# Performance work log

Measured on AMD Instinct MI355X. Metric: run time of the kernel, lower is better.

## Reference

```python
import jax, jax.numpy as jnp
import numpy as np

NTOKEN, EMBED, HID, VDIM, MAXLEN = 15000, 1024, 1024, 2048, 20
B, NOBJ = 128, 36

def gru_cell(x, h, Wih, Whh, bih, bhh):
    gi = x @ Wih.T + bih
    gh = h @ Whh.T + bhh
    i_r, i_z, i_n = jnp.split(gi, 3, axis=-1)
    h_r, h_z, h_n = jnp.split(gh, 3, axis=-1)
    r = jax.nn.sigmoid(i_r + h_r)
    z = jax.nn.sigmoid(i_z + h_z)
    n = jnp.tanh(i_n + r * h_n)
    return (1.0 - z) * n + z * h

def setup_inputs() -> dict:
    key = jax.random.key(0)
    ks = jax.random.split(key, 20)
    s = 0.02
    inp = {
        'v': jax.random.normal(ks[0], (B, NOBJ, VDIM), jnp.float32),
        'caption': jax.random.randint(ks[1], (B, MAXLEN), 0, NTOKEN, jnp.int32),
        'cap_len': jax.random.randint(ks[2], (B,), 2, MAXLEN + 1, jnp.int32),
        'emb': jax.random.normal(ks[3], (NTOKEN, EMBED), jnp.float32) * s,
        'Wih1': jax.random.normal(ks[4], (3 * HID, HID + VDIM + EMBED), jnp.float32) * s,
        'Whh1': jax.random.normal(ks[5], (3 * HID, HID), jnp.float32) * s,
        'bih1': jnp.zeros((3 * HID,), jnp.float32),
        'bhh1': jnp.zeros((3 * HID,), jnp.float32),
        'Wih2': jax.random.normal(ks[6], (3 * HID, VDIM + HID), jnp.float32) * s,
        'Whh2': jax.random.normal(ks[7], (3 * HID, HID), jnp.float32) * s,
        'bih2': jnp.zeros((3 * HID,), jnp.float32),
        'bhh2': jnp.zeros((3 * HID,), jnp.float32),
        'Wfc1': jax.random.normal(ks[8], (HID, HID), jnp.float32) * s,
        'bfc1': jnp.zeros((HID,), jnp.float32),
        'Wfc2': jax.random.normal(ks[9], (NTOKEN, HID), jnp.float32) * s,
        'bfc2': jnp.zeros((NTOKEN,), jnp.float32),
        'Wv': jax.random.normal(ks[10], (HID, VDIM), jnp.float32) * s,
        'bv': jnp.zeros((HID,), jnp.float32),
        'Wq': jax.random.normal(ks[11], (HID, HID), jnp.float32) * s,
        'bq': jnp.zeros((HID,), jnp.float32),
        'Wa': jax.random.normal(ks[12], (1, HID), jnp.float32) * s,
        'ba': jnp.zeros((1,), jnp.float32),
    }
    return inp

def reference(v, caption, cap_len, emb, Wih1, Whh1, bih1, bhh1, Wih2, Whh2, bih2, bhh2,
              Wfc1, bfc1, Wfc2, bfc2, Wv, bv, Wq, bq, Wa, ba):
    batch, num_objs, _ = v.shape
    # sort by descending caption length (stable, matching torch sort + inverse perm)
    sort_id = jnp.argsort(-cap_len)
    restore_id = jnp.argsort(sort_id)
    cap_len_s = cap_len[sort_id]
    sort_caption = caption[sort_id]
    v_s = v[sort_id]
    v_mean = v_s.mean(axis=1)                      # [B, VDIM]
    cap_emb = emb[sort_caption]                    # [B, T, E]
    # precompute attention v-projection (relu FCNet): [B, O, HID]
    v_proj = jax.nn.relu(jnp.einsum('bod,hd->boh', v_s, Wv) + bv)
    dec_len = cap_len_s - 1
    T = cap_emb.shape[1] - 1                       # max_len - 1 decode steps
    ts = jnp.arange(T)
    mask = (ts[:, None] < dec_len[None, :])        # [T, B]
    cap_seq = jnp.swapaxes(cap_emb[:, :T, :], 0, 1)  # [T, B, E]

    def step(carry, xs):
        h1, h2 = carry
        cap_t, m_t = xs
        x1 = jnp.concatenate([h2, v_mean, cap_t], axis=1)
        h1 = gru_cell(x1, h1, Wih1, Whh1, bih1, bhh1)
        h = h1 @ Wfc1.T + bfc1
        q_proj = jax.nn.relu(h @ Wq.T + bq)        # [B, HID]
        joint = v_proj * q_proj[:, None, :]        # [B, O, HID]
        logits = jnp.einsum('boh,h->bo', joint, Wa[0]) + ba[0]
        att = jax.nn.softmax(logits, axis=1)       # [B, O]
        att_v = jnp.einsum('bo,bod->bd', att, v_s)
        h2 = gru_cell(jnp.concatenate([att_v, h], axis=1), h2, Wih2, Whh2, bih2, bhh2)
        out_t = h2 @ Wfc2.T + bfc2                 # [B, NTOKEN]
        out_t = jnp.where(m_t[:, None], out_t, 0.0)
        alpha_t = jnp.where(m_t[:, None], att, 0.0)
        return (h1, h2), (out_t, alpha_t)

    h0 = jnp.zeros((batch, HID), v.dtype)
    (_, _), (outs, alphas) = jax.lax.scan(step, (h0, h0), (cap_seq, mask))
    # pad last timestep (loop never reaches t = max_len-1) and softmax all rows
    output = jnp.concatenate([jnp.swapaxes(outs, 0, 1),
                              jnp.zeros((batch, 1, Wfc2.shape[0]), v.dtype)], axis=1)
    alpha = jnp.concatenate([jnp.swapaxes(alphas, 0, 1),
                             jnp.zeros((batch, 1, num_objs), v.dtype)], axis=1)
    predict = jax.nn.softmax(output, axis=2)[restore_id]
    return predict, sort_caption[:, 1:], alpha[restore_id]
```

## Files before the change

kernel.cpp:

```cpp
#include <hip/hip_runtime.h>
#include <math.h>

#define NTOKEN 15000
#define EMBED  1024
#define HID    1024
#define VDIM   2048
#define MAXLEN 20
#define BATCH  128
#define NOBJ   36
#define TSTEP  19

typedef unsigned short ushort_t;
typedef __attribute__((ext_vector_type(8))) short short8;
typedef __attribute__((ext_vector_type(4))) float floatx4;

__device__ __forceinline__ float b2f(ushort_t u) {
    return __uint_as_float(((unsigned)u) << 16);
}
__device__ __forceinline__ ushort_t f2b(float f) {
    unsigned x = __float_as_uint(f);
    unsigned r = (x + 0x7fffu + ((x >> 16) & 1u)) >> 16;
    return (ushort_t)r;
}

template<int NF, bool OUT_BF16>
__device__ __forceinline__ void mfma_core(
    ushort_t* As, ushort_t* Bs,
    const ushort_t* __restrict__ A, int lda, const int* __restrict__ arow,
    const ushort_t* __restrict__ B, int ldb,
    void* __restrict__ Cv, int ldc, const int* __restrict__ crow,
    const float* __restrict__ bias, const float* __restrict__ mulvec,
    const float* __restrict__ cadd, long ldadd, int cadd_div,
    int relu_n, int N, int K, int m0, int n0, int k0)
{
    constexpr int ABUF = 128 * 40;
    constexpr int BBUF = NF * 16 * 40;
    const int tid  = threadIdx.x;
    const int lane = tid & 63;
    const int w    = tid >> 6;

    floatx4 acc[2][NF];
#pragma unroll
    for (int mf = 0; mf < 2; mf++)
#pragma unroll
        for (int nf = 0; nf < NF; nf++) acc[mf][nf] = (floatx4){0.f, 0.f, 0.f, 0.f};

    const int a_r = tid >> 1;
    const int a_c = (tid & 1) * 16;
    int a_g = m0 + a_r;
    if (arow) a_g = arow[a_g];
    const ushort_t* Aptr = A + (long)a_g * lda + k0 + a_c;

    int b_r, b_c;
    if constexpr (NF == 8)      { b_r = tid >> 1; b_c = (tid & 1) * 16; }
    else if constexpr (NF == 4) { b_r = tid >> 2; b_c = (tid & 3) * 8; }
    else                        { b_r = tid >> 3; b_c = (tid & 7) * 4; }
    int b_g = n0 + b_r;
    if (b_g >= N) b_g = N - 1;
    const ushort_t* Bptr = B + (long)b_g * ldb + k0 + b_c;

    const int fr = lane & 15;
    const int q8 = (lane >> 4) * 8;

    auto LDB = [&](uint4& v0, uint4& v1, int kof) {
        if constexpr (NF == 8) {
            v0 = *(const uint4*)(Bptr + kof);
            v1 = *(const uint4*)(Bptr + kof + 8);
        } else if constexpr (NF == 4) {
            v0 = *(const uint4*)(Bptr + kof);
        } else {
            uint2 t2 = *(const uint2*)(Bptr + kof);
            v0.x = t2.x; v0.y = t2.y;
        }
    };
    auto STA = [&](ushort_t* Asb, const uint4& v0, const uint4& v1) {
        *(uint4*)(Asb + a_r * 40 + a_c)     = v0;
        *(uint4*)(Asb + a_r * 40 + a_c + 8) = v1;
    };
    auto STB = [&](ushort_t* Bsb, const uint4& v0, const uint4& v1) {
        if constexpr (NF == 8) {
            *(uint4*)(Bsb + b_r * 40 + b_c)     = v0;
            *(uint4*)(Bsb + b_r * 40 + b_c + 8) = v1;
        } else if constexpr (NF == 4) {
            *(uint4*)(Bsb + b_r * 40 + b_c) = v0;
        } else {
            *(uint2*)(Bsb + b_r * 40 + b_c) = make_uint2(v0.x, v0.y);
        }
    };
    auto CMP = [&](const ushort_t* Asb, const ushort_t* Bsb) {
        short8 bfr[NF];
#pragma unroll
        for (int nf = 0; nf < NF; nf++)
            bfr[nf] = *(const short8*)(Bsb + (nf * 16 + fr) * 40 + q8);
#pragma unroll
        for (int mf = 0; mf < 2; mf++) {
            short8 af = *(const short8*)(Asb + (w * 32 + mf * 16 + fr) * 40 + q8);
#pragma unroll
            for (int nf = 0; nf < NF; nf++)
                acc[mf][nf] = __builtin_amdgcn_mfma_f32_16x16x32_bf16(
                    af, bfr[nf], acc[mf][nf], 0, 0, 0);
        }
    };

    const int T = K >> 5;

    uint4 ae0, ae1, ao0, ao1;
    uint4 be0, be1, bo0, bo1;
    ae0 = *(const uint4*)(Aptr);       ae1 = *(const uint4*)(Aptr + 8);
    LDB(be0, be1, 0);
    ao0 = *(const uint4*)(Aptr + 32);  ao1 = *(const uint4*)(Aptr + 40);
    LDB(bo0, bo1, 32);
    STA(As, ae0, ae1); STB(Bs, be0, be1);
    if (T > 2) {
        ae0 = *(const uint4*)(Aptr + 64); ae1 = *(const uint4*)(Aptr + 72);
        LDB(be0, be1, 64);
    }
    __syncthreads();

    for (int i = 0; i < T; i += 2) {
        STA(As + ABUF, ao0, ao1); STB(Bs + BBUF, bo0, bo1);
        if (i + 3 < T) {
            int kof = (i + 3) * 32;
            ao0 = *(const uint4*)(Aptr + kof); ao1 = *(const uint4*)(Aptr + kof + 8);
            LDB(bo0, bo1, kof);
        }
        CMP(As, Bs);
        __syncthreads();
        if (i + 2 < T) {
            STA(As, ae0, ae1); STB(Bs, be0, be1);
            if (i + 4 < T) {
                int kof = (i + 4) * 32;
                ae0 = *(const uint4*)(Aptr + kof); ae1 = *(const uint4*)(Aptr + kof + 8);
                LDB(be0, be1, kof);
            }
        }
        CMP(As + ABUF, Bs + BBUF);
        __syncthreads();
    }

    const int rq = lane >> 4;
#pragma unroll
    for (int mf = 0; mf < 2; mf++) {
#pragma unroll
        for (int r = 0; r < 4; r++) {
            int m = m0 + w * 32 + mf * 16 + rq * 4 + r;
            int cm = crow ? crow[m] : m;
            const float* caddrow = cadd ? (cadd + (long)(m / cadd_div) * ldadd) : nullptr;
#pragma unroll
            for (int nf = 0; nf < NF; nf++) {
                int n = n0 + nf * 16 + fr;
                if (n < N) {
                    float val = acc[mf][nf][r];
                    if (bias)    val += bias[n];
                    if (caddrow) val += caddrow[n];
                    if (n < relu_n) val = fmaxf(val, 0.f);
                    if (mulvec)  val *= mulvec[n];
                    if (OUT_BF16) ((ushort_t*)Cv)[(long)cm * ldc + n] = f2b(val);
                    else          ((float*)Cv)[(long)cm * ldc + n]   = val;
                }
            }
        }
    }
}

template<int NF, bool OUT_BF16>
__global__ __launch_bounds__(256) void mfma_gemm(
    const ushort_t* __restrict__ A, int lda, const int* __restrict__ arow,
    const ushort_t* __restrict__ B, int ldb,
    void* __restrict__ C, int ldc, const int* __restrict__ crow,
    const float* __restrict__ bias, const float* __restrict__ mulvec,
    const float* __restrict__ cadd, long ldadd, int cadd_div,
    int relu_n, int N, int K, int swz)
{
    __shared__ ushort_t As[2 * 128 * 40];
    __shared__ ushort_t Bs[2 * NF * 16 * 40];
    int mt = blockIdx.y, nt = blockIdx.x;
    if (swz) {
        int D = gridDim.x * gridDim.y;
        int d = blockIdx.y * gridDim.x + blockIdx.x;
        int x = d & 7, j = d >> 3, q = D >> 3, r = D & 7;
        int g = x * q + (x < r ? x : r) + j;
        mt = g % gridDim.y; nt = g / gridDim.y;
    }
    mfma_core<NF, OUT_BF16>(As, Bs, A, lda, arow, B, ldb, C, ldc, crow,
                            bias, mulvec, cadd, ldadd, cadd_div, relu_n,
                            N, K, mt * 128, nt * (NF * 16), 0);
}

template<int NF, int KS>
__global__ __launch_bounds__(256) void splitk_gemm(
    const ushort_t* __restrict__ A, int lda,
    const ushort_t* __restrict__ B, int ldb,
    float* __restrict__ C0, float* __restrict__ CP, long pstride, int ldc,
    const float* __restrict__ bias,
    const float* __restrict__ cadd, long ldadd,
    int N, int K)
{
    __shared__ ushort_t As[2 * 128 * 40];
    __shared__ ushort_t Bs[2 * NF * 16 * 40];
    const int s = blockIdx.y;
    const int Kc = K / KS;
    float* C = (s == 0) ? C0 : (CP + (long)(s - 1) * pstride);
    mfma_core<NF, false>(As, Bs, A, lda, nullptr, B, ldb, C, ldc, nullptr,
                         s == 0 ? bias : nullptr, nullptr,
                         s == 0 ? cadd : nullptr, ldadd, 1,
                         0, N, Kc, 0, blockIdx.x * (NF * 16), s * Kc);
}

template<int NF, int KS>
__global__ __launch_bounds__(256) void step3_kernel(
    const ushort_t* __restrict__ h1b, const ushort_t* __restrict__ h2b,
    const ushort_t* __restrict__ Wih1h, const ushort_t* __restrict__ Whh1b,
    const ushort_t* __restrict__ Whh2b,
    float* __restrict__ gi, float* __restrict__ gh, float* __restrict__ gh2,
    float* __restrict__ P_gi, float* __restrict__ P_gh, float* __restrict__ P_gh2,
    const float* __restrict__ gi1s_t,
    const float* __restrict__ bhh1, const float* __restrict__ bhh2)
{
    __shared__ ushort_t As[2 * 128 * 40];
    __shared__ ushort_t Bs[2 * NF * 16 * 40];
    const int s = blockIdx.y;
    const int Kc = 1024 / KS;
    const ushort_t* A; const ushort_t* B; float* C0; float* CP;
    const float* bias = nullptr; const float* cadd = nullptr;
    if (blockIdx.z == 0)      { A = h2b; B = Wih1h; C0 = gi;  CP = P_gi;  cadd = gi1s_t; }
    else if (blockIdx.z == 1) { A = h1b; B = Whh1b; C0 = gh;  CP = P_gh;  bias = bhh1; }
    else                      { A = h2b; B = Whh2b; C0 = gh2; CP = P_gh2; bias = bhh2; }
    float* C = (s == 0) ? C0 : (CP + (long)(s - 1) * 393216);
    mfma_core<NF, false>(As, Bs, A, 1024, nullptr, B, 1024, C, 3072, nullptr,
                         s == 0 ? bias : nullptr, nullptr,
                         s == 0 ? cadd : nullptr, (long)TSTEP * 3072, 1, 0,
                         3072, Kc, 0, blockIdx.x * (NF * 16), s * Kc);
}

__global__ void init_kernel(const int* __restrict__ caption,
                            int* __restrict__ tok_idx, int* __restrict__ crow20,
                            float* __restrict__ h12f, ushort_t* __restrict__ h12b)
{
    int idx = blockIdx.x * 256 + threadIdx.x;
    if (idx < BATCH * TSTEP) {
        int b = idx / TSTEP, t = idx % TSTEP;
        tok_idx[idx] = caption[b * MAXLEN + t];
        crow20[idx]  = b * MAXLEN + t;
    }
    h12f[idx] = 0.f;
    h12b[idx] = 0;
}

__global__ void sort_caption_kernel(const int* __restrict__ caption,
                                    const int* __restrict__ cap_len,
                                    float* __restrict__ out1)
{
    int i = threadIdx.x;
    if (i < BATCH) {
        int li = cap_len[i];
        int rank = 0;
        for (int j = 0; j < BATCH; j++) {
            int lj = cap_len[j];
            if (lj > li || (lj == li && j < i)) rank++;
        }
        for (int k = 0; k < TSTEP; k++)
            out1[rank * TSTEP + k] = (float)caption[i * MAXLEN + 1 + k];
    }
}

__global__ void vmean_kernel(const float* __restrict__ v,
                             float* __restrict__ vmean, ushort_t* __restrict__ vmeanb)
{
    int idx = blockIdx.x * 256 + threadIdx.x;
    int b = idx >> 11, d = idx & (VDIM - 1);
    float s = 0.f;
    for (int o = 0; o < NOBJ; o++) s += v[((long)b * NOBJ + o) * VDIM + d];
    float m = s * (1.0f / 36.0f);
    vmean[idx] = m;
    vmeanb[idx] = f2b(m);
}

__global__ void conv_kernel(const float* __restrict__ src, long ld,
                            const int* __restrict__ rowidx,
                            ushort_t* __restrict__ dst, int rows, int cols)
{
    long idx4 = ((long)blockIdx.x * 256 + threadIdx.x) * 4;
    if (idx4 >= (long)rows * cols) return;
    int r = (int)(idx4 / cols);
    int c = (int)(idx4 % cols);
    long sr = rowidx ? rowidx[r] : r;
    float4 f = *(const float4*)(src + sr * ld + c);
    dst[idx4 + 0] = f2b(f.x);
    dst[idx4 + 1] = f2b(f.y);
    dst[idx4 + 2] = f2b(f.z);
    dst[idx4 + 3] = f2b(f.w);
}

__global__ void transpose_conv_kernel(const float* __restrict__ src,
                                      ushort_t* __restrict__ dst)
{
    __shared__ float tile[32][33];
    int bx = blockIdx.x, by = blockIdx.y;
    int lx = threadIdx.x & 31, ly = threadIdx.x >> 5;
    for (int i = 0; i < 32; i += 8)
        tile[ly + i][lx] = src[(long)(by * 32 + ly + i) * 1024 + bx * 32 + lx];
    __syncthreads();
    for (int i = 0; i < 32; i += 8)
        dst[(long)(bx * 32 + ly + i) * 1024 + by * 32 + lx] = f2b(tile[lx][ly + i]);
}

__global__ void bias_fold_kernel(const float* __restrict__ Wq,
                                 const float* __restrict__ Wih2,
                                 const float* __restrict__ bfc1,
                                 const float* __restrict__ bq,
                                 const float* __restrict__ bih2,
                                 float* __restrict__ bcat2)
{
    int wave = blockIdx.x * 4 + (threadIdx.x >> 6);
    int lane = threadIdx.x & 63;
    for (int n = wave; n < 4096; n += 256) {
        const float* wrow = (n < 1024) ? (Wq + (long)n * 1024)
                                       : (Wih2 + (long)(n - 1024) * 3072 + 2048);
        float s = 0.f;
        for (int j = lane; j < 1024; j += 64) s += wrow[j] * bfc1[j];
        for (int off = 32; off > 0; off >>= 1) s += __shfl_down(s, off);
        if (lane == 0) bcat2[n] = s + ((n < 1024) ? bq[n] : bih2[n - 1024]);
    }
}

__global__ void gru_kernel(const float* __restrict__ gi, const float* __restrict__ giP,
                           const float* __restrict__ gh, const float* __restrict__ ghP,
                           int nsp,
                           float* __restrict__ h, ushort_t* __restrict__ hb,
                           ushort_t* __restrict__ hstore, int t)
{
    int idx = blockIdx.x * 256 + threadIdx.x;
    int b = idx >> 10, j = idx & (HID - 1);
    long o0 = (long)b * 3 * HID + j;
    float ir = gi[o0], iz = gi[o0 + HID], in_ = gi[o0 + 2 * HID];
    float hr = gh[o0], hz = gh[o0 + HID], hn  = gh[o0 + 2 * HID];
    for (int s = 0; s < nsp; s++) {
        const float* gp = giP + (long)s * 393216;
        const float* hp = ghP + (long)s * 393216;
        ir  += gp[o0]; iz += gp[o0 + HID]; in_ += gp[o0 + 2 * HID];
        hr  += hp[o0]; hz += hp[o0 + HID]; hn  += hp[o0 + 2 * HID];
    }
    float r = 1.f / (1.f + expf(-(ir + hr)));
    float z = 1.f / (1.f + expf(-(iz + hz)));
    float n = tanhf(in_ + r * hn);
    float hnew = (1.f - z) * n + z * h[idx];
    h[idx] = hnew;
    ushort_t hq = f2b(hnew);
    hb[idx] = hq;
    if (hstore) hstore[((long)(b * TSTEP + t) << 10) | j] = hq;
}

__global__ __launch_bounds__(512) void attn_gru2_kernel(
    const ushort_t* __restrict__ vwb, const float* __restrict__ qgi2,
    const float* __restrict__ qP,
    const ushort_t* __restrict__ vwih2,
    const float* __restrict__ gh2, const float* __restrict__ ghP2,
    const int* __restrict__ cap_len, int t,
    float* __restrict__ h2, ushort_t* __restrict__ h2b,
    ushort_t* __restrict__ hstore, float* __restrict__ alpha)
{
    int b = blockIdx.x;
    __shared__ float qs[HID];
    __shared__ float att_s[NOBJ];
    __shared__ float gis[3 * HID];
    int tid = threadIdx.x, lane = tid & 63, w = tid >> 6;
    const float* qb = qgi2 + (long)b * 4096;

    for (int hh = tid; hh < HID; hh += 512) {
        float s = qb[hh];
        for (int sp = 0; sp < 3; sp++) s += qP[(long)sp * 524288 + (long)b * 4096 + hh];
        qs[hh] = fmaxf(s, 0.f);
    }
    __syncthreads();

    for (int o = w; o < NOBJ; o += 8) {
        const ushort_t* vwo = vwb + ((long)b * NOBJ + o) * HID;
        float s = 0.f;
        for (int hh = lane; hh < HID; hh += 64) s += b2f(vwo[hh]) * qs[hh];
        for (int off = 32; off > 0; off >>= 1) s += __shfl_down(s, off);
        if (lane == 0) att_s[o] = s;
    }
    __syncthreads();
    if (tid == 0) {
        float mx = att_s[0];
        for (int o = 1; o < NOBJ; o++) mx = fmaxf(mx, att_s[o]);
        float sum = 0.f;
        for (int o = 0; o < NOBJ; o++) { float e = expf(att_s[o] - mx); att_s[o] = e; sum += e; }
        float inv = 1.f / sum;
        for (int o = 0; o < NOBJ; o++) att_s[o] *= inv;
    }
    __syncthreads();
    bool m = (t < cap_len[b] - 1);
    if (tid < NOBJ) alpha[((long)b * MAXLEN + t) * NOBJ + tid] = m ? att_s[tid] : 0.f;

    const ushort_t* vw2 = vwih2 + (long)b * NOBJ * 3072;
    for (int j = tid; j < 3 * HID; j += 512) {
        float s = qb[HID + j];
        for (int sp = 0; sp < 3; sp++) s += qP[(long)sp * 524288 + (long)b * 4096 + HID + j];
        for (int o = 0; o < NOBJ; o++) s += att_s[o] * b2f(vw2[(long)o * 3072 + j]);
        gis[j] = s;
    }
    __syncthreads();

    for (int j = tid; j < HID; j += 512) {
        long o0 = (long)b * 3 * HID + j;
        float hr = gh2[o0], hz = gh2[o0 + HID], hn = gh2[o0 + 2 * HID];
        for (int sp = 0; sp < 3; sp++) {
            const float* hp = ghP2 + (long)sp * 393216;
            hr += hp[o0]; hz += hp[o0 + HID]; hn += hp[o0 + 2 * HID];
        }
        float ir = gis[j], iz = gis[HID + j], in_ = gis[2 * HID + j];
        float r = 1.f / (1.f + expf(-(ir + hr)));
        float z = 1.f / (1.f + expf(-(iz + hz)));
        float n = tanhf(in_ + r * hn);
        int idx = (b << 10) | j;
        float hnew = (1.f - z) * n + z * h2[idx];
        h2[idx] = hnew;
        ushort_t hq = f2b(hnew);
        h2b[idx] = hq;
        hstore[((long)(b * TSTEP + t) << 10) | j] = hq;
    }
}

__global__ __launch_bounds__(256) void softmax_kernel(float* __restrict__ predict,
                                                      float* __restrict__ alpha,
                                                      const int* __restrict__ cap_len)
{
    __shared__ float ls[NTOKEN];
    __shared__ float sred[4];
    int row = blockIdx.x;
    int b = row / MAXLEN, t = row % MAXLEN;
    float* p = predict + (long)row * NTOKEN;
    int tid = threadIdx.x;
    int dec = cap_len[b] - 1;
    if (t >= dec) {
        const float u = 1.0f / (float)NTOKEN;
        for (int i = tid; i < NTOKEN; i += 256) p[i] = u;
        if (t == MAXLEN - 1 && tid < NOBJ) alpha[(long)row * NOBJ + tid] = 0.f;
        return;
    }
    float mx = -3.4e38f;
    for (int i = tid; i < NTOKEN; i += 256) {
        float x = p[i]; ls[i] = x; mx = fmaxf(mx, x);
    }
    for (int off = 32; off > 0; off >>= 1) mx = fmaxf(mx, __shfl_down(mx, off));
    if ((tid & 63) == 0) sred[tid >> 6] = mx;
    __syncthreads();
    mx = fmaxf(fmaxf(sred[0], sred[1]), fmaxf(sred[2], sred[3]));
    __syncthreads();
    float s = 0.f;
    for (int i = tid; i < NTOKEN; i += 256) {
        float e = expf(ls[i] - mx); ls[i] = e; s += e;
    }
    for (int off = 32; off > 0; off >>= 1) s += __shfl_down(s, off);
    if ((tid & 63) == 0) sred[tid >> 6] = s;
    __syncthreads();
    s = sred[0] + sred[1] + sred[2] + sred[3];
    float inv = 1.f / s;
    for (int i = tid; i < NTOKEN; i += 256) p[i] = ls[i] * inv;
}

extern "C" void kernel_launch(void* const* d_in, const int* in_sizes, int n_in,
                              void* d_out, int out_size, void* d_ws, size_t ws_size,
                              hipStream_t stream)
{
    const float* v       = (const float*)d_in[0];
    const int*   caption = (const int*)  d_in[1];
    const int*   cap_len = (const int*)  d_in[2];
    const float* emb     = (const float*)d_in[3];
    const float* Wih1    = (const float*)d_in[4];
    const float* Whh1    = (const float*)d_in[5];
    const float* bih1    = (const float*)d_in[6];
    const float* bhh1    = (const float*)d_in[7];
    const float* Wih2    = (const float*)d_in[8];
    const float* Whh2    = (const float*)d_in[9];
    const float* bih2    = (const float*)d_in[10];
    const float* bhh2    = (const float*)d_in[11];
    const float* Wfc1    = (const float*)d_in[12];
    const float* bfc1    = (const float*)d_in[13];
    const float* Wfc2    = (const float*)d_in[14];
    const float* bfc2    = (const float*)d_in[15];
    const float* Wv      = (const float*)d_in[16];
    const float* bv      = (const float*)d_in[17];
    const float* Wq      = (const float*)d_in[18];
    const float* bq      = (const float*)d_in[19];
    const float* Wa      = (const float*)d_in[20];

    float* f32base = (float*)d_ws;
    float* gvm   = f32base;
    float* gi1s  = gvm   + 393216;
    float* h1    = gi1s  + 7471104;
    float* h2    = h1    + 131072;
    float* gi    = h2    + 131072;
    float* gh    = gi    + 393216;
    float* gh2   = gh    + 393216;
    float* qgi2  = gh2   + 393216;
    float* vmean = qgi2  + 524288;
    float* bcat2 = vmean + 262144;
    ushort_t* ub = (ushort_t*)(bcat2 + 4096);
    ushort_t* Wih1h = ub;
    ushort_t* Wih1c = Wih1h + 3145728;
    ushort_t* Whh1b = Wih1c + 3145728;
    ushort_t* Whh2b = Whh1b + 3145728;
    ushort_t* Wih2v = Whh2b + 3145728;
    ushort_t* Wcat2 = Wih2v + 6291456;
    ushort_t* Wfc2b = Wcat2 + 4194304;
    ushort_t* vw_bf = Wfc2b + 15360000;
    ushort_t* H2Ab  = vw_bf + 4718592;
    ushort_t* h1b   = H2Ab  + 2490368;
    ushort_t* h2b   = h1b   + 131072;
    ushort_t* x2v   = h2b   + 131072;
    ushort_t* vmeanb= x2v   + 262144;
    ushort_t* TEMP  = vmeanb+ 262144;
    ushort_t* vwih2 = Wfc2b;
    ushort_t* vb     = TEMP;
    ushort_t* Wvb    = TEMP + 9437184;
    ushort_t* Wqb    = TEMP;
    ushort_t* Wih2hb = TEMP + 1048576;
    ushort_t* Wfc1T  = TEMP + 4194304;
    ushort_t* Wih1m  = TEMP;
    ushort_t* Acap   = TEMP;
    float* TEMPf  = (float*)TEMP;
    float* P_gi   = TEMPf;
    float* P_gh   = P_gi  + 3 * 393216;
    float* P_gh2  = P_gh  + 3 * 393216;
    float* P_q    = P_gh2 + 3 * 393216;
    int* tok_idx = (int*)(TEMP + 11534336);
    int* crow20  = tok_idx + BATCH * TSTEP;

    float* out     = (float*)d_out;
    float* predict = out;
    float* out1    = out + (long)BATCH * MAXLEN * NTOKEN;
    float* alpha   = out1 + (long)BATCH * TSTEP;

    #define CONV(src, ld, rowidx, dst, rows, cols) \
        conv_kernel<<<(int)(((long)(rows)*(cols)/4 + 255)/256), 256, 0, stream>>>( \
            src, ld, rowidx, dst, rows, cols)

    init_kernel<<<1024, 256, 0, stream>>>(caption, tok_idx, crow20, h1, h1b);
    sort_caption_kernel<<<1, 128, 0, stream>>>(caption, cap_len, out1);
    vmean_kernel<<<(BATCH * VDIM) / 256, 256, 0, stream>>>(v, vmean, vmeanb);

    CONV(Wih1,        4096, nullptr, Wih1h, 3072, 1024);
    CONV(Wih1 + 3072, 4096, nullptr, Wih1c, 3072, 1024);
    CONV(Whh1,        1024, nullptr, Whh1b, 3072, 1024);
    CONV(Whh2,        1024, nullptr, Whh2b, 3072, 1024);
    CONV(Wih2,        3072, nullptr, Wih2v, 3072, 2048);

    CONV(v,  2048, nullptr, vb,  4608, 2048);
    CONV(Wv, 2048, nullptr, Wvb, 1024, 2048);
    mfma_gemm<8, true><<<dim3(8, 36), 256, 0, stream>>>(
        vb, 2048, nullptr, Wvb, 2048, vw_bf, 1024, nullptr,
        bv, Wa, nullptr, 0, 1, 1024, 1024, 2048, 1);

    mfma_gemm<8, true><<<dim3(24, 36), 256, 0, stream>>>(
        vb, 2048, nullptr, Wih2v, 2048, vwih2, 3072, nullptr,
        nullptr, nullptr, nullptr, 0, 1, 0, 3072, 2048, 1);

    CONV(Wq,          1024, nullptr, Wqb,    1024, 1024);
    CONV(Wih2 + 2048, 3072, nullptr, Wih2hb, 3072, 1024);
    transpose_conv_kernel<<<dim3(32, 32), 256, 0, stream>>>(Wfc1, Wfc1T);
    mfma_gemm<8, true><<<dim3(8, 8), 256, 0, stream>>>(
        Wqb, 1024, nullptr, Wfc1T, 1024, Wcat2, 1024, nullptr,
        nullptr, nullptr, nullptr, 0, 1, 0, 1024, 1024, 1);
    mfma_gemm<8, true><<<dim3(8, 24), 256, 0, stream>>>(
        Wih2hb, 1024, nullptr, Wfc1T, 1024, Wcat2 + 1048576, 1024, nullptr,
        nullptr, nullptr, nullptr, 0, 1, 0, 1024, 1024, 1);
    bias_fold_kernel<<<64, 256, 0, stream>>>(Wq, Wih2, bfc1, bq, bih2, bcat2);

    CONV(Wih1 + 1024, 4096, nullptr, Wih1m, 3072, 2048);
    mfma_gemm<8, false><<<dim3(24, 1), 256, 0, stream>>>(
        vmeanb, 2048, nullptr, Wih1m, 2048, gvm, 3072, nullptr,
        bih1, nullptr, nullptr, 0, 1, 0, 3072, 2048, 0);

    CONV(emb, 1024, tok_idx, Acap, 2432, 1024);
    mfma_gemm<8, false><<<dim3(24, 19), 256, 0, stream>>>(
        Acap, 1024, nullptr, Wih1c, 1024, gi1s, 3072, nullptr,
        nullptr, nullptr, gvm, 3072, TSTEP, 0, 3072, 1024, 1);

    for (int t = 0; t < TSTEP; t++) {
        step3_kernel<2, 4><<<dim3(96, 4, 3), 256, 0, stream>>>(
            h1b, h2b, Wih1h, Whh1b, Whh2b, gi, gh, gh2,
            P_gi, P_gh, P_gh2, gi1s + (long)t * 3072, bhh1, bhh2);
        gru_kernel<<<512, 256, 0, stream>>>(gi, P_gi, gh, P_gh, 3, h1, h1b, nullptr, t);
        splitk_gemm<2, 4><<<dim3(128, 4), 256, 0, stream>>>(
            h1b, 1024, Wcat2, 1024, qgi2, P_q, 524288, 4096,
            bcat2, nullptr, 0, 4096, 1024);
        attn_gru2_kernel<<<BATCH, 512, 0, stream>>>(
            vw_bf, qgi2, P_q, vwih2, gh2, P_gh2, cap_len, t,
            h2, h2b, H2Ab, alpha);
    }

    CONV(Wfc2, 1024, nullptr, Wfc2b, NTOKEN, 1024);
    mfma_gemm<8, false><<<dim3(118, 19), 256, 0, stream>>>(
        H2Ab, 1024, nullptr, Wfc2b, 1024, predict, NTOKEN, crow20,
        bfc2, nullptr, nullptr, 0, 1, 0, NTOKEN, 1024, 1);
    softmax_kernel<<<BATCH * MAXLEN, 256, 0, stream>>>(predict, alpha, cap_len);
    #undef CONV
}
```

Before: 2.357 ms.

## Stage GEMM tiles with direct global-to-LDS loads and XOR swizzle; vectorize attention loops

The shared MFMA GEMM core now loads A and B tiles straight from global memory into LDS with global_load_lds, replacing the register-staged double buffer. The padded stride-40 layout becomes a stride-32 layout with an XOR swizzle to avoid bank conflicts. This is meant to cut register pressure and LDS store instructions on the GEMM path, but the pipeline now prefetches only one stage ahead. Separately, the attention kernel's object dot products and attention-weighted value accumulation use 8-wide vector loads instead of scalar loads.

```diff
diff --git a/kernel.cpp b/kernel.cpp
--- a/kernel.cpp
+++ b/kernel.cpp
@@ -21,6 +21,12 @@
     unsigned x = __float_as_uint(f);
     unsigned r = (x + 0x7fffu + ((x >> 16) & 1u)) >> 16;
     return (ushort_t)r;
+}
+
+__device__ __forceinline__ void gload16(const ushort_t* g, ushort_t* l) {
+    __builtin_amdgcn_global_load_lds(
+        (const __attribute__((address_space(1))) unsigned int*)g,
+        (__attribute__((address_space(3))) unsigned int*)l, 16, 0, 0);
 }
 
 template<int NF, bool OUT_BF16>
@@ -33,8 +39,8 @@
     const float* __restrict__ cadd, long ldadd, int cadd_div,
     int relu_n, int N, int K, int m0, int n0, int k0)
 {
-    constexpr int ABUF = 128 * 40;
-    constexpr int BBUF = NF * 16 * 40;
+    constexpr int ABUF = 128 * 32;
+    constexpr int BBUF = NF * 16 * 32;
     const int tid  = threadIdx.x;
     const int lane = tid & 63;
     const int w    = tid >> 6;
@@ -45,56 +51,57 @@
 #pragma unroll
         for (int nf = 0; nf < NF; nf++) acc[mf][nf] = (floatx4){0.f, 0.f, 0.f, 0.f};
 
-    const int a_r = tid >> 1;
-    const int a_c = (tid & 1) * 16;
-    int a_g = m0 + a_r;
-    if (arow) a_g = arow[a_g];
-    const ushort_t* Aptr = A + (long)a_g * lda + k0 + a_c;
-
-    int b_r, b_c;
-    if constexpr (NF == 8)      { b_r = tid >> 1; b_c = (tid & 1) * 16; }
-    else if constexpr (NF == 4) { b_r = tid >> 2; b_c = (tid & 3) * 8; }
-    else                        { b_r = tid >> 3; b_c = (tid & 7) * 4; }
-    int b_g = n0 + b_r;
-    if (b_g >= N) b_g = N - 1;
-    const ushort_t* Bptr = B + (long)b_g * ldb + k0 + b_c;
-
-    const int fr = lane & 15;
-    const int q8 = (lane >> 4) * 8;
-
-    auto LDB = [&](uint4& v0, uint4& v1, int kof) {
+    const int sr = lane >> 2;
+    const int sc = lane & 3;
+
+    int ra0 = w * 32 + sr;
+    int ra1 = ra0 + 16;
+    int ga0 = m0 + ra0; if (arow) ga0 = arow[ga0];
+    int ga1 = m0 + ra1; if (arow) ga1 = arow[ga1];
+    const ushort_t* srcA0 = A + (long)ga0 * lda + k0 + ((sc ^ (ra0 & 3)) * 8);
+    const ushort_t* srcA1 = A + (long)ga1 * lda + k0 + ((sc ^ (ra1 & 3)) * 8);
+
+    const ushort_t* srcB0;
+    const ushort_t* srcB1 = nullptr;
+    if constexpr (NF == 8) {
+        int rb0 = w * 32 + sr, rb1 = rb0 + 16;
+        int gb0 = n0 + rb0; if (gb0 >= N) gb0 = N - 1;
+        int gb1 = n0 + rb1; if (gb1 >= N) gb1 = N - 1;
+        srcB0 = B + (long)gb0 * ldb + k0 + ((sc ^ (rb0 & 3)) * 8);
+        srcB1 = B + (long)gb1 * ldb + k0 + ((sc ^ (rb1 & 3)) * 8);
+    } else {
+        int rb0 = w * 16 + sr;
+        int gb0 = n0 + rb0; if (gb0 >= N) gb0 = N - 1;
+        srcB0 = B + (long)gb0 * ldb + k0 + ((sc ^ (rb0 & 3)) * 8);
+    }
+
+    ushort_t* Abase = As + w * 1024;
+    ushort_t* Bbase = (NF == 8) ? (Bs + w * 1024) : (Bs + w * 512);
+
+    auto STAGE = [&](int p, int kk) {
+        gload16(srcA0 + kk, Abase + p * ABUF);
+        gload16(srcA1 + kk, Abase + p * ABUF + 512);
         if constexpr (NF == 8) {
-            v0 = *(const uint4*)(Bptr + kof);
-            v1 = *(const uint4*)(Bptr + kof + 8);
+            gload16(srcB0 + kk, Bbase + p * BBUF);
+            gload16(srcB1 + kk, Bbase + p * BBUF + 512);
         } else if constexpr (NF == 4) {
-            v0 = *(const uint4*)(Bptr + kof);
+            gload16(srcB0 + kk, Bbase + p * BBUF);
         } else {
-            uint2 t2 = *(const uint2*)(Bptr + kof);
-            v0.x = t2.x; v0.y = t2.y;
+            if (w < 2) gload16(srcB0 + kk, Bbase + p * BBUF);
         }
     };
-    auto STA = [&](ushort_t* Asb, const uint4& v0, const uint4& v1) {
-        *(uint4*)(Asb + a_r * 40 + a_c)     = v0;
-        *(uint4*)(Asb + a_r * 40 + a_c + 8) = v1;
-    };
-    auto STB = [&](ushort_t* Bsb, const uint4& v0, const uint4& v1) {
-        if constexpr (NF == 8) {
-            *(uint4*)(Bsb + b_r * 40 + b_c)     = v0;
-            *(uint4*)(Bsb + b_r * 40 + b_c + 8) = v1;
-        } else if constexpr (NF == 4) {
-            *(uint4*)(Bsb + b_r * 40 + b_c) = v0;
-        } else {
-            *(uint2*)(Bsb + b_r * 40 + b_c) = make_uint2(v0.x, v0.y);
-        }
-    };
-    auto CMP = [&](const ushort_t* Asb, const ushort_t* Bsb) {
+
+    const int fr   = lane & 15;
+    const int aoff = (((lane >> 4) ^ (fr & 3)) * 8);
+
+    auto CMP = [&](const ushort_t* Ap, const ushort_t* Bp) {
         short8 bfr[NF];
 #pragma unroll
         for (int nf = 0; nf < NF; nf++)
-            bfr[nf] = *(const short8*)(Bsb + (nf * 16 + fr) * 40 + q8);
+            bfr[nf] = *(const short8*)(Bp + (nf * 16 + fr) * 32 + aoff);
 #pragma unroll
         for (int mf = 0; mf < 2; mf++) {
-            short8 af = *(const short8*)(Asb + (w * 32 + mf * 16 + fr) * 40 + q8);
+            short8 af = *(const short8*)(Ap + (w * 32 + mf * 16 + fr) * 32 + aoff);
 #pragma unroll
             for (int nf = 0; nf < NF; nf++)
                 acc[mf][nf] = __builtin_amdgcn_mfma_f32_16x16x32_bf16(
@@ -103,39 +110,14 @@
     };
 
     const int T = K >> 5;
-
-    uint4 ae0, ae1, ao0, ao1;
-    uint4 be0, be1, bo0, bo1;
-    ae0 = *(const uint4*)(Aptr);       ae1 = *(const uint4*)(Aptr + 8);
-    LDB(be0, be1, 0);
-    ao0 = *(const uint4*)(Aptr + 32);  ao1 = *(const uint4*)(Aptr + 40);
-    LDB(bo0, bo1, 32);
-    STA(As, ae0, ae1); STB(Bs, be0, be1);
-    if (T > 2) {
-        ae0 = *(const uint4*)(Aptr + 64); ae1 = *(const uint4*)(Aptr + 72);
-        LDB(be0, be1, 64);
-    }
-    __syncthreads();
-
-    for (int i = 0; i < T; i += 2) {
-        STA(As + ABUF, ao0, ao1); STB(Bs + BBUF, bo0, bo1);
-        if (i + 3 < T) {
-            int kof = (i + 3) * 32;
-            ao0 = *(const uint4*)(Aptr + kof); ao1 = *(const uint4*)(Aptr + kof + 8);
-            LDB(bo0, bo1, kof);
-        }
-        CMP(As, Bs);
+    STAGE(0, 0);
+    __syncthreads();
+    int p = 0;
+    for (int i = 0; i < T; i++) {
+        if (i + 1 < T) STAGE(p ^ 1, (i + 1) * 32);
+        CMP(As + p * ABUF, Bs + p * BBUF);
         __syncthreads();
-        if (i + 2 < T) {
-            STA(As, ae0, ae1); STB(Bs, be0, be1);
-            if (i + 4 < T) {
-                int kof = (i + 4) * 32;
-                ae0 = *(const uint4*)(Aptr + kof); ae1 = *(const uint4*)(Aptr + kof + 8);
-                LDB(be0, be1, kof);
-            }
-        }
-        CMP(As + ABUF, Bs + BBUF);
-        __syncthreads();
+        p ^= 1;
     }
 
     const int rq = lane >> 4;
@@ -172,8 +154,8 @@
     const float* __restrict__ cadd, long ldadd, int cadd_div,
     int relu_n, int N, int K, int swz)
 {
-    __shared__ ushort_t As[2 * 128 * 40];
-    __shared__ ushort_t Bs[2 * NF * 16 * 40];
+    __shared__ ushort_t As[2 * 128 * 32];
+    __shared__ ushort_t Bs[2 * NF * 16 * 32];
     int mt = blockIdx.y, nt = blockIdx.x;
     if (swz) {
         int D = gridDim.x * gridDim.y;
@@ -196,8 +178,8 @@
     const float* __restrict__ cadd, long ldadd,
     int N, int K)
 {
-    __shared__ ushort_t As[2 * 128 * 40];
-    __shared__ ushort_t Bs[2 * NF * 16 * 40];
+    __shared__ ushort_t As[2 * 128 * 32];
+    __shared__ ushort_t Bs[2 * NF * 16 * 32];
     const int s = blockIdx.y;
     const int Kc = K / KS;
     float* C = (s == 0) ? C0 : (CP + (long)(s - 1) * pstride);
@@ -217,8 +199,8 @@
     const float* __restrict__ gi1s_t,
     const float* __restrict__ bhh1, const float* __restrict__ bhh2)
 {
-    __shared__ ushort_t As[2 * 128 * 40];
-    __shared__ ushort_t Bs[2 * NF * 16 * 40];
+    __shared__ ushort_t As[2 * 128 * 32];
+    __shared__ ushort_t Bs[2 * NF * 16 * 32];
     const int s = blockIdx.y;
     const int Kc = 1024 / KS;
     const ushort_t* A; const ushort_t* B; float* C0; float* CP;
@@ -377,7 +359,11 @@
     for (int o = w; o < NOBJ; o += 8) {
         const ushort_t* vwo = vwb + ((long)b * NOBJ + o) * HID;
         float s = 0.f;
-        for (int hh = lane; hh < HID; hh += 64) s += b2f(vwo[hh]) * qs[hh];
+        for (int hh = lane * 8; hh < HID; hh += 512) {
+            short8 v8 = *(const short8*)(vwo + hh);
+#pragma unroll
+            for (int k = 0; k < 8; k++) s += b2f((ushort_t)v8[k]) * qs[hh + k];
+        }
         for (int off = 32; off > 0; off >>= 1) s += __shfl_down(s, off);
         if (lane == 0) att_s[o] = s;
     }
@@ -395,11 +381,27 @@
     if (tid < NOBJ) alpha[((long)b * MAXLEN + t) * NOBJ + tid] = m ? att_s[tid] : 0.f;
 
     const ushort_t* vw2 = vwih2 + (long)b * NOBJ * 3072;
-    for (int j = tid; j < 3 * HID; j += 512) {
-        float s = qb[HID + j];
-        for (int sp = 0; sp < 3; sp++) s += qP[(long)sp * 524288 + (long)b * 4096 + HID + j];
-        for (int o = 0; o < NOBJ; o++) s += att_s[o] * b2f(vw2[(long)o * 3072 + j]);
-        gis[j] = s;
+    for (int j0 = tid * 8; j0 < 3 * HID; j0 += 512 * 8) {
+        float sv[8];
+        float4 qa = *(const float4*)(qb + HID + j0);
+        float4 qc = *(const float4*)(qb + HID + j0 + 4);
+        sv[0] = qa.x; sv[1] = qa.y; sv[2] = qa.z; sv[3] = qa.w;
+        sv[4] = qc.x; sv[5] = qc.y; sv[6] = qc.z; sv[7] = qc.w;
+        for (int sp = 0; sp < 3; sp++) {
+            const float* qpp = qP + (long)sp * 524288 + (long)b * 4096 + HID + j0;
+            float4 pa = *(const float4*)(qpp);
+            float4 pc = *(const float4*)(qpp + 4);
+            sv[0] += pa.x; sv[1] += pa.y; sv[2] += pa.z; sv[3] += pa.w;
+            sv[4] += pc.x; sv[5] += pc.y; sv[6] += pc.z; sv[7] += pc.w;
+        }
+        for (int o = 0; o < NOBJ; o++) {
+            float a = att_s[o];
+            short8 v8 = *(const short8*)(vw2 + (long)o * 3072 + j0);
+#pragma unroll
+            for (int k = 0; k < 8; k++) sv[k] += a * b2f((ushort_t)v8[k]);
+        }
+#pragma unroll
+        for (int k = 0; k < 8; k++) gis[j0 + k] = sv[k];
     }
     __syncthreads();
 
```

Measured after the change: 1.934 ms. 18.0% less time.
